# Kernel tuning notes

Measured on AMD Instinct MI355X. Metric: run time of the kernel, lower is better.

## Reference

```python
import jax, jax.numpy as jnp
import numpy as np

C = 0.01          # curvature
EPS = 1e-6        # eps used in midpoint / weight normalization (matches torch code)
MIN_NORM = 1e-10  # numerical floor for norms
BALL_EPS = 1e-5   # projection margin


def _norm(x):
    return jnp.sqrt(jnp.clip(jnp.sum(x * x, axis=-1, keepdims=True), MIN_NORM))


def log_map_zero(x, c):
    sc = jnp.sqrt(c)
    n = _norm(x)
    return jnp.arctanh(jnp.clip(sc * n, -1.0 + BALL_EPS, 1.0 - BALL_EPS)) * x / (sc * n)


def exp_map_zero(v, c):
    sc = jnp.sqrt(c)
    n = _norm(v)
    return jnp.tanh(sc * n) * v / (sc * n)


def project_to_ball(x, c):
    n = _norm(x)
    maxn = (1.0 - BALL_EPS) / jnp.sqrt(c)
    return jnp.where(n > maxn, x * (maxn / n), x)


def mobius_add(x, y, c):
    x2 = jnp.sum(x * x, axis=-1, keepdims=True)
    y2 = jnp.sum(y * y, axis=-1, keepdims=True)
    xy = jnp.sum(x * y, axis=-1, keepdims=True)
    num = (1.0 + 2.0 * c * xy + c * y2) * x + (1.0 - c * x2) * y
    den = 1.0 + 2.0 * c * xy + (c * c) * x2 * y2
    return num / jnp.clip(den, MIN_NORM)


def setup_inputs() -> dict:
    N, E, R, D = 50000, 400000, 230, 16
    key = jax.random.key(0)
    ks = jax.random.split(key, 8)
    h_hyper = project_to_ball(0.1 * jax.random.normal(ks[0], (N, D), dtype=jnp.float32), C)
    node_norm = jax.random.uniform(ks[1], (N, 1), dtype=jnp.float32)
    xav = float(np.sqrt(2.0 / (D + D)))
    rel_weight = xav * jax.random.normal(ks[2], (R, D, D), dtype=jnp.float32)
    loop_weight = xav * jax.random.normal(ks[3], (D, D), dtype=jnp.float32)
    rel_emb = 0.1 * jax.random.normal(ks[4], (R, D), dtype=jnp.float32)
    src = jax.random.randint(ks[5], (E,), 0, N, dtype=jnp.int32)
    dst = jax.random.randint(ks[6], (E,), 0, N, dtype=jnp.int32)
    etype = jax.random.randint(ks[7], (E,), 0, R, dtype=jnp.int32)
    return {"h_hyper": h_hyper, "node_norm": node_norm, "rel_weight": rel_weight,
            "loop_weight": loop_weight, "rel_emb": rel_emb,
            "src": src, "dst": dst, "etype": etype}


def reference(h_hyper, node_norm, rel_weight, loop_weight, rel_emb, src, dst, etype):
    c = C
    N = h_hyper.shape[0]
    # --- msg_func: Mobius matvec per edge (log -> gathered GEMM -> +rel -> exp) ---
    h_tan = log_map_zero(h_hyper, c)                                  # [N, D]
    msg_tan = jnp.einsum('ei,eio->eo', h_tan[src], rel_weight[etype])  # [E, D]
    msg_tan = msg_tan + rel_emb[etype]
    msg = exp_map_zero(msg_tan, c)                                    # [E, D]
    # --- reduce_func: Einstein midpoint per destination node ---
    en = node_norm[dst, 0]                                            # [E] per-edge dst norm
    norm_sum = jax.ops.segment_sum(en, dst, num_segments=N)           # [N]
    w = en / (norm_sum[dst] + EPS)                                    # normalized weights
    lam = 2.0 / (1.0 - c * jnp.sum(msg * msg, axis=-1) + EPS)         # Lorentz factors [E]
    wl = w * lam
    numer = jax.ops.segment_sum(wl[:, None] * msg, dst, num_segments=N)  # [N, D]
    denom = jax.ops.segment_sum(wl, dst, num_segments=N) + EPS           # [N]
    h_agg = project_to_ball(numer / denom[:, None], c)
    # --- self loop in tangent space, combined with Mobius addition ---
    loop_hyp = exp_map_zero(h_tan @ loop_weight, c)
    h_new = mobius_add(h_agg, loop_hyp, c)
    return h_new
```

## Files before the change

kernel.cpp:

```cpp
#include <hip/hip_runtime.h>

#define C_CURV   0.01f
#define SQRT_C   0.1f
#define EPS_W    1e-6f
#define MIN_NORM 1e-10f
#define BALL_EPS 1e-5f
#define CAP      64

typedef __attribute__((ext_vector_type(4))) float f32x4;

__device__ __forceinline__ float fast_rcp(float x)  { return __builtin_amdgcn_rcpf(x); }
__device__ __forceinline__ float fast_sqrt(float x) { return __builtin_amdgcn_sqrtf(x); }
__device__ __forceinline__ float tanh_over_x(float x) {
    float t = __expf(2.0f * x);
    return (t - 1.0f) * fast_rcp((t + 1.0f) * x);
}

__device__ __forceinline__ float group4_sum(float v) {
    v += __shfl_xor(v, 1, 4);
    v += __shfl_xor(v, 2, 4);
    return v;
}
__device__ __forceinline__ float group16_sum(float v) {
    v += __shfl_xor(v, 1, 16);
    v += __shfl_xor(v, 2, 16);
    v += __shfl_xor(v, 4, 16);
    v += __shfl_xor(v, 8, 16);
    return v;
}

__global__ __launch_bounds__(256) void fhnn_prep(
        const float* __restrict__ h_hyper,
        const float* __restrict__ loop_weight,
        float* __restrict__ h_tan,
        float* __restrict__ loop_hyp,
        int*   __restrict__ cursor,
        int    nZero4,
        int N, int blocksN) {
    if ((int)blockIdx.x >= blocksN) {
        int i = (blockIdx.x - blocksN) * blockDim.x + threadIdx.x;
        if (i < nZero4) ((int4*)cursor)[i] = make_int4(0, 0, 0, 0);
        return;
    }
    __shared__ float Wl[256];
    Wl[threadIdx.x] = loop_weight[threadIdx.x];
    __syncthreads();

    int gid = blockIdx.x * blockDim.x + threadIdx.x;
    int t = gid >> 2, j = gid & 3;
    if (t >= N) return;

    f32x4 x = ((const f32x4*)h_hyper)[gid];

    float sq  = group4_sum(x.x * x.x + x.y * x.y + x.z * x.z + x.w * x.w);
    float n   = fast_sqrt(fmaxf(sq, MIN_NORM));
    float scn = SQRT_C * n;
    float z   = fminf(scn, 1.0f - BALL_EPS);
    float at  = 0.5f * __logf((1.0f + z) * fast_rcp(1.0f - z));
    float s   = at * fast_rcp(scn);
    f32x4 ht  = x * s;
    ((f32x4*)h_tan)[gid] = ht;

    f32x4 acc = (f32x4)(0.0f);
    #pragma unroll
    for (int q = 0; q < 4; ++q) {
        float h0 = __shfl(ht.x, q, 4);
        float h1 = __shfl(ht.y, q, 4);
        float h2 = __shfl(ht.z, q, 4);
        float h3 = __shfl(ht.w, q, 4);
        const f32x4* Wrow = (const f32x4*)Wl;
        acc += h0 * Wrow[(4 * q + 0) * 4 + j];
        acc += h1 * Wrow[(4 * q + 1) * 4 + j];
        acc += h2 * Wrow[(4 * q + 2) * 4 + j];
        acc += h3 * Wrow[(4 * q + 3) * 4 + j];
    }
    float sq2  = group4_sum(acc.x * acc.x + acc.y * acc.y + acc.z * acc.z + acc.w * acc.w);
    float n2   = fast_sqrt(fmaxf(sq2, MIN_NORM));
    float f2   = tanh_over_x(SQRT_C * n2);
    ((f32x4*)loop_hyp)[gid] = acc * f2;
}

__global__ __launch_bounds__(256) void fhnn_scatter(
        const int* __restrict__ src,
        const int* __restrict__ dst,
        const int* __restrict__ etype,
        int*      __restrict__ cursor,
        unsigned* __restrict__ bucket,
        int E) {
    int e = blockIdx.x * blockDim.x + threadIdx.x;
    if (e >= E) return;
    int t = dst[e];
    int slot = atomicAdd(&cursor[t], 1);
    if (slot < CAP)
        bucket[t * CAP + slot] = (unsigned)src[e] | ((unsigned)etype[e] << 16);
}

__global__ __launch_bounds__(256) void fhnn_reduce(
        const float*    __restrict__ h_tan,
        const float*    __restrict__ rel_weight,
        const float*    __restrict__ rel_emb,
        const unsigned* __restrict__ bucket,
        const int*      __restrict__ cursor,
        const float*    __restrict__ node_norm,
        const float*    __restrict__ loop_hyp,
        float*          __restrict__ out,
        int N) {
    int wid  = (blockIdx.x * blockDim.x + threadIdx.x) >> 6;
    int lane = threadIdx.x & 63;
    if (wid >= N) return;
    int t = wid;
    int slot = lane >> 4, jj = lane & 15;

    int cn = min(cursor[t], CAP);

    float accM = 0.0f;
    float accL = 0.0f;
    for (int k = slot; k < cn; k += 4) {
        unsigned pk = bucket[t * CAP + k];
        int s = (int)(pk & 0xFFFFu);
        int r = (int)(pk >> 16);
        float ht = h_tan[s * 16 + jj];
        const float* W = rel_weight + (size_t)r * 256;
        float acc = 0.0f;
        #pragma unroll
        for (int i = 0; i < 16; ++i) {
            float hi = __shfl(ht, i, 16);
            acc = fmaf(hi, W[i * 16 + jj], acc);
        }
        float v  = acc + rel_emb[r * 16 + jj];
        float sq = group16_sum(v * v);
        float f  = tanh_over_x(SQRT_C * fast_sqrt(fmaxf(sq, MIN_NORM)));
        float m2 = f * f * sq;
        float lam = 2.0f * fast_rcp(1.0f - C_CURV * m2 + EPS_W);
        accM = fmaf(v, f * lam, accM);
        accL += lam;
    }
    accM += __shfl_xor(accM, 16, 64);
    accM += __shfl_xor(accM, 32, 64);
    accL += __shfl_xor(accL, 16, 64);
    accL += __shfl_xor(accL, 32, 64);

    float en    = node_norm[t];
    float wsc   = en * fast_rcp((float)cn * en + EPS_W);
    float denom = wsc * accL + EPS_W;
    float rs    = wsc * fast_rcp(denom);
    float x     = accM * rs;

    float x2 = group16_sum(x * x);
    float n  = fast_sqrt(fmaxf(x2, MIN_NORM));
    const float maxn = (1.0f - BALL_EPS) / SQRT_C;
    float scale = (n > maxn) ? (maxn * fast_rcp(n)) : 1.0f;
    x *= scale;

    float y   = loop_hyp[t * 16 + jj];
    float x2p = group16_sum(x * x);
    float y2  = group16_sum(y * y);
    float xy  = group16_sum(x * y);

    float a   = 1.0f + 2.0f * C_CURV * xy + C_CURV * y2;
    float b   = 1.0f - C_CURV * x2p;
    float num = a * x + b * y;
    float d2  = 1.0f + 2.0f * C_CURV * xy + C_CURV * C_CURV * x2p * y2;
    if (lane < 16)
        out[t * 16 + jj] = num * fast_rcp(fmaxf(d2, MIN_NORM));
}

extern "C" void kernel_launch(void* const* d_in, const int* in_sizes, int n_in,
                              void* d_out, int out_size, void* d_ws, size_t ws_size,
                              hipStream_t stream) {
    const float* h_hyper     = (const float*)d_in[0];
    const float* node_norm   = (const float*)d_in[1];
    const float* rel_weight  = (const float*)d_in[2];
    const float* loop_weight = (const float*)d_in[3];
    const float* rel_emb     = (const float*)d_in[4];
    const int*   src         = (const int*)d_in[5];
    const int*   dst         = (const int*)d_in[6];
    const int*   etype       = (const int*)d_in[7];

    const int N = in_sizes[1];
    const int E = in_sizes[5];

    char* ws = (char*)d_ws;
    size_t offs = 0;
    auto alloc = [&](size_t bytes) -> void* {
        void* p = ws + offs;
        offs += (bytes + 255) & ~(size_t)255;
        return p;
    };
    float*    h_tan    = (float*)alloc((size_t)N * 16 * 4);
    float*    loop_hyp = (float*)alloc((size_t)N * 16 * 4);
    unsigned* bucket   = (unsigned*)alloc((size_t)N * CAP * 4);
    int*      cursor   = (int*)alloc((size_t)N * 4);
    int nZero4 = (int)(N + 3) >> 2;

    const int threads = 256;
    int blocksN4 = (N * 4 + threads - 1) / threads;
    int blocksZ  = (nZero4 + threads - 1) / threads;
    int blocksE1 = (E + threads - 1) / threads;
    int blocksR  = (N + 3) / 4;

    fhnn_prep<<<blocksN4 + blocksZ, threads, 0, stream>>>(
        h_hyper, loop_weight, h_tan, loop_hyp, cursor, nZero4, N, blocksN4);
    fhnn_scatter<<<blocksE1, threads, 0, stream>>>(src, dst, etype, cursor, bucket, E);
    fhnn_reduce<<<blocksR, threads, 0, stream>>>(
        h_tan, rel_weight, rel_emb, bucket, cursor, node_norm, loop_hyp, (float*)d_out, N);
}
```

Measured before the change: 75.39 us.

## Remap reduce kernel to 4 lanes per edge with float4 vector math

Each edge in the reduce kernel is now handled by 4 lanes, each owning 4 output columns as float4 vectors, instead of 16 lanes owning one column each. A wavefront therefore processes 16 edges at once rather than 4. The per-edge matvec uses direct vector loads of the full source row and weight columns in place of 16 cross-lane shuffles, and norms need only 2 shuffle steps. In exchange each lane reloads the whole h_tan row and uses more registers, and the final cross-slot reduction has more shuffle steps.

```diff
diff --git a/kernel.cpp b/kernel.cpp
--- a/kernel.cpp
+++ b/kernel.cpp
@@ -17,15 +17,8 @@
 }
 
 __device__ __forceinline__ float group4_sum(float v) {
-    v += __shfl_xor(v, 1, 4);
-    v += __shfl_xor(v, 2, 4);
-    return v;
-}
-__device__ __forceinline__ float group16_sum(float v) {
-    v += __shfl_xor(v, 1, 16);
-    v += __shfl_xor(v, 2, 16);
-    v += __shfl_xor(v, 4, 16);
-    v += __shfl_xor(v, 8, 16);
+    v += __shfl_xor(v, 1, 64);
+    v += __shfl_xor(v, 2, 64);
     return v;
 }
 
@@ -109,60 +102,72 @@
     int lane = threadIdx.x & 63;
     if (wid >= N) return;
     int t = wid;
-    int slot = lane >> 4, jj = lane & 15;
+    int slot = lane >> 2, j = lane & 3;
 
     int cn = min(cursor[t], CAP);
 
-    float accM = 0.0f;
+    f32x4 accM = (f32x4)(0.0f);
     float accL = 0.0f;
-    for (int k = slot; k < cn; k += 4) {
+    for (int k = slot; k < cn; k += 16) {
         unsigned pk = bucket[t * CAP + k];
         int s = (int)(pk & 0xFFFFu);
         int r = (int)(pk >> 16);
-        float ht = h_tan[s * 16 + jj];
-        const float* W = rel_weight + (size_t)r * 256;
-        float acc = 0.0f;
-        #pragma unroll
-        for (int i = 0; i < 16; ++i) {
-            float hi = __shfl(ht, i, 16);
-            acc = fmaf(hi, W[i * 16 + jj], acc);
-        }
-        float v  = acc + rel_emb[r * 16 + jj];
-        float sq = group16_sum(v * v);
+
+        const f32x4* h4 = (const f32x4*)(h_tan + (size_t)s * 16);
+        f32x4 h0 = h4[0], h1 = h4[1], h2 = h4[2], h3 = h4[3];
+
+        const f32x4* W4 = (const f32x4*)(rel_weight + (size_t)r * 256);
+        f32x4 a = (f32x4)(0.0f);
+        a += h0.x * W4[ 0 * 4 + j];  a += h0.y * W4[ 1 * 4 + j];
+        a += h0.z * W4[ 2 * 4 + j];  a += h0.w * W4[ 3 * 4 + j];
+        a += h1.x * W4[ 4 * 4 + j];  a += h1.y * W4[ 5 * 4 + j];
+        a += h1.z * W4[ 6 * 4 + j];  a += h1.w * W4[ 7 * 4 + j];
+        a += h2.x * W4[ 8 * 4 + j];  a += h2.y * W4[ 9 * 4 + j];
+        a += h2.z * W4[10 * 4 + j];  a += h2.w * W4[11 * 4 + j];
+        a += h3.x * W4[12 * 4 + j];  a += h3.y * W4[13 * 4 + j];
+        a += h3.z * W4[14 * 4 + j];  a += h3.w * W4[15 * 4 + j];
+
+        f32x4 v = a + ((const f32x4*)(rel_emb + (size_t)r * 16))[j];
+
+        float sq = group4_sum(v.x * v.x + v.y * v.y + v.z * v.z + v.w * v.w);
         float f  = tanh_over_x(SQRT_C * fast_sqrt(fmaxf(sq, MIN_NORM)));
         float m2 = f * f * sq;
         float lam = 2.0f * fast_rcp(1.0f - C_CURV * m2 + EPS_W);
-        accM = fmaf(v, f * lam, accM);
+        accM += v * (f * lam);
         accL += lam;
     }
-    accM += __shfl_xor(accM, 16, 64);
-    accM += __shfl_xor(accM, 32, 64);
-    accL += __shfl_xor(accL, 16, 64);
-    accL += __shfl_xor(accL, 32, 64);
+    #pragma unroll
+    for (int m = 4; m <= 32; m <<= 1) {
+        accM.x += __shfl_xor(accM.x, m, 64);
+        accM.y += __shfl_xor(accM.y, m, 64);
+        accM.z += __shfl_xor(accM.z, m, 64);
+        accM.w += __shfl_xor(accM.w, m, 64);
+        accL   += __shfl_xor(accL,   m, 64);
+    }
 
     float en    = node_norm[t];
     float wsc   = en * fast_rcp((float)cn * en + EPS_W);
     float denom = wsc * accL + EPS_W;
     float rs    = wsc * fast_rcp(denom);
-    float x     = accM * rs;
-
-    float x2 = group16_sum(x * x);
+    f32x4 x     = accM * rs;
+
+    float x2 = group4_sum(x.x * x.x + x.y * x.y + x.z * x.z + x.w * x.w);
     float n  = fast_sqrt(fmaxf(x2, MIN_NORM));
     const float maxn = (1.0f - BALL_EPS) / SQRT_C;
     float scale = (n > maxn) ? (maxn * fast_rcp(n)) : 1.0f;
     x *= scale;
 
-    float y   = loop_hyp[t * 16 + jj];
-    float x2p = group16_sum(x * x);
-    float y2  = group16_sum(y * y);
-    float xy  = group16_sum(x * y);
-
-    float a   = 1.0f + 2.0f * C_CURV * xy + C_CURV * y2;
-    float b   = 1.0f - C_CURV * x2p;
-    float num = a * x + b * y;
+    f32x4 y   = ((const f32x4*)(loop_hyp + (size_t)t * 16))[j];
+    float x2p = group4_sum(x.x * x.x + x.y * x.y + x.z * x.z + x.w * x.w);
+    float y2  = group4_sum(y.x * y.x + y.y * y.y + y.z * y.z + y.w * y.w);
+    float xy  = group4_sum(x.x * y.x + x.y * y.y + x.z * y.z + x.w * y.w);
+
+    float a1  = 1.0f + 2.0f * C_CURV * xy + C_CURV * y2;
+    float b1  = 1.0f - C_CURV * x2p;
+    f32x4 num = a1 * x + b1 * y;
     float d2  = 1.0f + 2.0f * C_CURV * xy + C_CURV * C_CURV * x2p * y2;
-    if (lane < 16)
-        out[t * 16 + jj] = num * fast_rcp(fmaxf(d2, MIN_NORM));
+    if (slot == 0)
+        ((f32x4*)out)[t * 4 + j] = num * fast_rcp(fmaxf(d2, MIN_NORM));
 }
 
 extern "C" void kernel_launch(void* const* d_in, const int* in_sizes, int n_in,
```

Measured after the change: 73.19 us. 1.03x faster.
